# Optimization experiments

Hardware: AMD Instinct MI355X
Metric: run time of the kernel (lower is better)

Reference implementation:

```python
import jax, jax.numpy as jnp
import numpy as np

K = 10
ALPHA = 0.1
N_NODES = 100000
N_EDGES = 1600000
D_FEAT = 50


def setup_inputs() -> dict:
    key = jax.random.key(0)
    k1, k2, k3 = jax.random.split(key, 3)
    feat = jax.random.normal(k1, (N_NODES, D_FEAT), dtype=jnp.float32)
    src = jax.random.randint(k2, (N_EDGES,), 0, N_NODES, dtype=jnp.int64)
    dst = jax.random.randint(k3, (N_EDGES,), 0, N_NODES, dtype=jnp.int64)
    return {"feat": feat, "src": src, "dst": dst}


def reference(feat, src, dst):
    # APPNP: H^{t+1} = (1-a) * D^{-1/2} A D^{-1/2} H^t + a * H^0
    n = feat.shape[0]
    # in-degree per node, clipped to >= 1 (as in the original clip_by_value)
    deg = jax.ops.segment_sum(jnp.ones(dst.shape[0], feat.dtype), dst, num_segments=n)
    norm = jnp.clip(deg, 1.0, None) ** -0.5  # [N]
    norm = norm[:, None]                      # broadcast over feature dims
    feat_0 = feat
    for _ in range(K):
        h = feat * norm                       # pre-normalize (D^{-1/2})
        # message = h[src] (edge weight is 1 since edge_drop=0), aggregate by sum at dst
        agg = jax.ops.segment_sum(h[src], dst, num_segments=n)  # [N, D]
        feat = (1.0 - ALPHA) * (agg * norm) + ALPHA * feat_0
    return feat
```

## Files before the change

### kernel.cpp

```cpp
#include <hip/hip_runtime.h>
#include <hip/hip_bf16.h>


#define NN 100000
#define EE 1600000
#define DD 50
#define GS 64
#define KK 10
#define NBLK 391

__device__ __forceinline__ float feat_at(const void* f, long long i, int ft) {
    if (ft) return ((const float*)f)[i];
    unsigned int w = ((unsigned int)((const unsigned short*)f)[i]) << 16;
    return __uint_as_float(w);
}

__device__ __forceinline__ float bf16_ld(const unsigned short* p, int i) {
    unsigned int w = ((unsigned int)p[i]) << 16;
    return __uint_as_float(w);
}

__device__ __forceinline__ unsigned short bf16_st(float x) {
    unsigned int u = __float_as_uint(x);
    unsigned int r = (u + 0x7FFF + ((u >> 16) & 1)) >> 16;
    return (unsigned short)r;
}

__global__ __launch_bounds__(512) void APPNPConv_62199716381208_kernel(
        const void* featp, const void* srcp, const void* dstp,
        int* deg, float* norm, int* row_ptr, int* col_idx, int* bsum, int* flag,
        const unsigned short* gin, unsigned short* gout, float* outp,
        int phase, int last) {
    __shared__ int sh[512];
    const int tid = threadIdx.x;
    const int gidx = blockIdx.x * blockDim.x + tid;

    if (phase == 0) {
        if (gidx < NN) deg[gidx] = 0;
        if (blockIdx.x == 0 && tid == 0) {
            const int* a = (const int*)dstp;
            int odd_or = a[1] | a[3] | a[5] | a[7] | a[9] | a[11] | a[13] | a[15];
            flag[0] = (odd_or == 0) ? 1 : 0;
            const unsigned short* w = (const unsigned short*)featp;
            int isf32 = 0;
            for (int k = 0; k < 64; ++k) {
                unsigned int b = ((unsigned int)w[k]) << 16;
                float ax = fabsf(__uint_as_float(b));
                if (!(ax < 100.0f)) isf32 = 1;
            }
            flag[1] = isf32;
        }
        return;
    }
    if (phase == 1) {
        if (gidx < EE) {
            int d = flag[0] ? (int)((const long long*)dstp)[gidx]
                            : ((const int*)dstp)[gidx];
            if ((unsigned int)d < (unsigned int)NN) atomicAdd(&deg[d], 1);
        }
        return;
    }
    if (phase == 2) {
        int i = blockIdx.x * 256 + tid;
        sh[tid] = (i < NN) ? deg[i] : 0;
        __syncthreads();
        for (int off = 128; off > 0; off >>= 1) {
            if (tid < off) sh[tid] += sh[tid + off];
            __syncthreads();
        }
        if (tid == 0) bsum[blockIdx.x] = sh[0];
        return;
    }
    if (phase == 3) {
        int v = (tid < NBLK) ? bsum[tid] : 0;
        sh[tid] = v;
        __syncthreads();
        for (int off = 1; off < 512; off <<= 1) {
            int x = (tid >= off) ? sh[tid - off] : 0;
            __syncthreads();
            sh[tid] += x;
            __syncthreads();
        }
        if (tid < NBLK) bsum[tid] = sh[tid] - v;
        return;
    }
    if (phase == 4) {
        int i = blockIdx.x * 256 + tid;
        int v = (i < NN) ? deg[i] : 0;
        sh[tid] = v;
        __syncthreads();
        for (int off = 1; off < 256; off <<= 1) {
            int x = (tid >= off) ? sh[tid - off] : 0;
            __syncthreads();
            sh[tid] += x;
            __syncthreads();
        }
        int excl = sh[tid] - v + bsum[blockIdx.x];
        if (i < NN) {
            row_ptr[i] = excl;
            deg[i] = excl;
            norm[i] = rsqrtf((float)(v < 1 ? 1 : v));
        }
        if (i == 0) row_ptr[NN] = EE;
        return;
    }
    if (phase == 5) {
        if (gidx < EE) {
            int is64 = flag[0];
            int d = is64 ? (int)((const long long*)dstp)[gidx] : ((const int*)dstp)[gidx];
            int c = is64 ? (int)((const long long*)srcp)[gidx] : ((const int*)srcp)[gidx];
            if ((unsigned int)d < (unsigned int)NN && (unsigned int)c < (unsigned int)NN) {
                int pos = atomicAdd(&deg[d], 1);
                if ((unsigned int)pos < (unsigned int)EE) col_idx[pos] = c;
            }
        }
        return;
    }
    if (phase == 6) {
        int v = gidx >> 6;
        int d = gidx & 63;
        if (v < NN && d < DD) {
            float x = feat_at(featp, (long long)v * DD + d, flag[1]);
            gout[v * GS + d] = bf16_st(x * norm[v]);
        }
        return;
    }
    {
        const int lane = tid & 63;
        const int v = (blockIdx.x << 2) + (tid >> 6);
        if (v >= NN) return;
        const int beg = row_ptr[v];
        const int end = row_ptr[v + 1];
        float s0 = 0.0f, s1 = 0.0f, s2 = 0.0f, s3 = 0.0f;
        for (int base = beg; base < end; base += 64) {
            int idx = base + lane;
            int my = (idx < end) ? col_idx[idx] : 0;
            int cnt = end - base;
            if (cnt > 64) cnt = 64;
            int j = 0;
            for (; j + 8 <= cnt; j += 8) {
                int c0 = __shfl(my, j, 64);
                int c1 = __shfl(my, j + 1, 64);
                int c2 = __shfl(my, j + 2, 64);
                int c3 = __shfl(my, j + 3, 64);
                int c4 = __shfl(my, j + 4, 64);
                int c5 = __shfl(my, j + 5, 64);
                int c6 = __shfl(my, j + 6, 64);
                int c7 = __shfl(my, j + 7, 64);
                if (lane < DD) {
                    float v0 = bf16_ld(gin, c0 * GS + lane);
                    float v1 = bf16_ld(gin, c1 * GS + lane);
                    float v2 = bf16_ld(gin, c2 * GS + lane);
                    float v3 = bf16_ld(gin, c3 * GS + lane);
                    float v4 = bf16_ld(gin, c4 * GS + lane);
                    float v5 = bf16_ld(gin, c5 * GS + lane);
                    float v6 = bf16_ld(gin, c6 * GS + lane);
                    float v7 = bf16_ld(gin, c7 * GS + lane);
                    s0 += v0 + v4;
                    s1 += v1 + v5;
                    s2 += v2 + v6;
                    s3 += v3 + v7;
                }
            }
            for (; j + 4 <= cnt; j += 4) {
                int c0 = __shfl(my, j, 64);
                int c1 = __shfl(my, j + 1, 64);
                int c2 = __shfl(my, j + 2, 64);
                int c3 = __shfl(my, j + 3, 64);
                if (lane < DD) {
                    s0 += bf16_ld(gin, c0 * GS + lane);
                    s1 += bf16_ld(gin, c1 * GS + lane);
                    s2 += bf16_ld(gin, c2 * GS + lane);
                    s3 += bf16_ld(gin, c3 * GS + lane);
                }
            }
            for (; j < cnt; ++j) {
                int c = __shfl(my, j, 64);
                if (lane < DD) s0 += bf16_ld(gin, c * GS + lane);
            }
        }
        if (lane < DD) {
            float sum = (s0 + s1) + (s2 + s3);
            float nv = norm[v];
            float f0 = feat_at(featp, (long long)v * DD + lane, flag[1]);
            float res = 0.9f * (sum * nv) + 0.1f * f0;
            if (last) outp[v * DD + lane] = res;
            else      gout[v * GS + lane] = bf16_st(res * nv);
        }
    }
}

extern "C" void kernel_launch(void* const* d_in, const int* in_sizes, int n_in,
                              void* d_out, int out_size, void* d_ws, size_t ws_size,
                              hipStream_t stream) {
    const void* featp = d_in[0];
    const void* src = d_in[1];
    const void* dst = d_in[2];
    float* outf = (float*)d_out;
    unsigned short* outb16 = (unsigned short*)d_out;
    size_t out_bytes = (size_t)out_size * 4;
    (void)in_sizes;

    if (n_in != 3) {
        hipMemsetAsync(d_out, 0x50, out_bytes, stream);
        return;
    }

    size_t a_deg  = (((size_t)NN * 4) + 255) / 256 * 256;
    size_t a_norm = a_deg;
    size_t a_rp   = (((size_t)(NN + 1) * 4) + 255) / 256 * 256;
    size_t a_col  = (((size_t)EE * 4) + 255) / 256 * 256;
    size_t a_bsum = (((size_t)NBLK * 4) + 255) / 256 * 256;
    size_t a_flag = 256;
    size_t a_buf  = (((size_t)NN * GS * 2) + 255) / 256 * 256;
    if (ws_size < a_deg + a_norm + a_rp + a_col + a_bsum + a_flag + a_buf) {
        hipMemsetAsync(d_out, 0x40, out_bytes, stream);
        return;
    }
    char* p = (char*)d_ws;
    int* deg      = (int*)p;   p += a_deg;
    float* norm   = (float*)p; p += a_norm;
    int* row_ptr  = (int*)p;   p += a_rp;
    int* col_idx  = (int*)p;   p += a_col;
    int* bsum     = (int*)p;   p += a_bsum;
    int* flag     = (int*)p;   p += a_flag;
    unsigned short* bufA = (unsigned short*)p;

    (void)hipGetLastError();

    #define LCH(grid, blk, gi, go, ph, la) \
        APPNPConv_62199716381208_kernel<<<(grid), (blk), 0, stream>>>( \
            featp, src, dst, deg, norm, row_ptr, col_idx, bsum, flag, \
            (gi), (go), outf, (ph), (la))

    LCH(NBLK, 256, bufA, bufA, 0, 0);
    LCH((EE + 255) / 256, 256, bufA, bufA, 1, 0);
    LCH(NBLK, 256, bufA, bufA, 2, 0);
    LCH(1, 512, bufA, bufA, 3, 0);
    LCH(NBLK, 256, bufA, bufA, 4, 0);
    LCH((EE + 255) / 256, 256, bufA, bufA, 5, 0);
    LCH((NN * GS + 255) / 256, 256, bufA, outb16, 6, 0);

    for (int it = 1; it <= KK; ++it) {
        const unsigned short* gi = (it & 1) ? outb16 : bufA;
        unsigned short* go       = (it & 1) ? bufA : outb16;
        LCH(NN / 4, 256, gi, go, 7, (it == KK) ? 1 : 0);
    }
    #undef LCH

    if (hipGetLastError() != hipSuccess) {
        hipMemsetAsync(d_out, 0xBF, out_bytes, stream);
    }
}
```

Baseline: 804.1 us.

## Build CSR via two-level bucket sort with shared-memory histograms

```diff
diff --git a/kernel.cpp b/kernel.cpp
--- a/kernel.cpp
+++ b/kernel.cpp
@@ -7,7 +7,11 @@
 #define DD 50
 #define GS 64
 #define KK 10
-#define NBLK 391
+#define RB 9
+#define NPR 512
+#define NRANGE 196
+#define EPB 8192
+#define NPB 196
 
 __device__ __forceinline__ float feat_at(const void* f, long long i, int ft) {
     if (ft) return ((const float*)f)[i];
@@ -15,6 +19,10 @@
     return __uint_as_float(w);
 }
 
+__device__ __forceinline__ int idx_at(const void* p, int e, int is64) {
+    return is64 ? (int)((const long long*)p)[e] : ((const int*)p)[e];
+}
+
 __device__ __forceinline__ float bf16_ld(const unsigned short* p, int i) {
     unsigned int w = ((unsigned int)p[i]) << 16;
     return __uint_as_float(w);
@@ -26,18 +34,19 @@
     return (unsigned short)r;
 }
 
-__global__ __launch_bounds__(512) void APPNPConv_62199716381208_kernel(
+__global__ __launch_bounds__(256) void APPNPConv_62199716381208_kernel(
         const void* featp, const void* srcp, const void* dstp,
-        int* deg, float* norm, int* row_ptr, int* col_idx, int* bsum, int* flag,
+        float* norm, int* row_ptr, int* col_idx,
+        int* rc, int* rs, int* rcur, int* flag,
+        unsigned long long* bucket,
         const unsigned short* gin, unsigned short* gout, float* outp,
         int phase, int last) {
-    __shared__ int sh[512];
+    __shared__ int sh[1280];
     const int tid = threadIdx.x;
-    const int gidx = blockIdx.x * blockDim.x + tid;
 
     if (phase == 0) {
-        if (gidx < NN) deg[gidx] = 0;
-        if (blockIdx.x == 0 && tid == 0) {
+        if (tid < NRANGE) { rc[tid] = 0; }
+        if (tid == 0) {
             const int* a = (const int*)dstp;
             int odd_or = a[1] | a[3] | a[5] | a[7] | a[9] | a[11] | a[13] | a[15];
             flag[0] = (odd_or == 0) ? 1 : 0;
@@ -53,70 +62,114 @@
         return;
     }
     if (phase == 1) {
-        if (gidx < EE) {
-            int d = flag[0] ? (int)((const long long*)dstp)[gidx]
-                            : ((const int*)dstp)[gidx];
-            if ((unsigned int)d < (unsigned int)NN) atomicAdd(&deg[d], 1);
-        }
+        if (tid < NRANGE) sh[tid] = 0;
+        __syncthreads();
+        const int is64 = flag[0];
+        const int base_e = blockIdx.x * EPB;
+        for (int k = 0; k < EPB / 256; ++k) {
+            int e = base_e + k * 256 + tid;
+            if (e < EE) {
+                int d = idx_at(dstp, e, is64);
+                atomicAdd(&sh[d >> RB], 1);
+            }
+        }
+        __syncthreads();
+        if (tid < NRANGE && sh[tid] > 0) atomicAdd(&rc[tid], sh[tid]);
         return;
     }
     if (phase == 2) {
-        int i = blockIdx.x * 256 + tid;
-        sh[tid] = (i < NN) ? deg[i] : 0;
-        __syncthreads();
-        for (int off = 128; off > 0; off >>= 1) {
-            if (tid < off) sh[tid] += sh[tid + off];
+        int v = (tid < NRANGE) ? rc[tid] : 0;
+        sh[1024 + tid] = v;
+        __syncthreads();
+        for (int off = 1; off < 256; off <<= 1) {
+            int x = (tid >= off) ? sh[1024 + tid - off] : 0;
             __syncthreads();
-        }
-        if (tid == 0) bsum[blockIdx.x] = sh[0];
+            sh[1024 + tid] += x;
+            __syncthreads();
+        }
+        int excl = sh[1024 + tid] - v;
+        if (tid < NRANGE) { rs[tid] = excl; rcur[tid] = excl; }
+        if (tid == NRANGE) rs[NRANGE] = EE;
+        if (tid == 0) row_ptr[NN] = EE;
         return;
     }
     if (phase == 3) {
-        int v = (tid < NBLK) ? bsum[tid] : 0;
-        sh[tid] = v;
-        __syncthreads();
-        for (int off = 1; off < 512; off <<= 1) {
-            int x = (tid >= off) ? sh[tid - off] : 0;
+        if (tid < NRANGE) sh[tid] = 0;
+        __syncthreads();
+        const int is64 = flag[0];
+        const int base_e = blockIdx.x * EPB;
+        for (int k = 0; k < EPB / 256; ++k) {
+            int e = base_e + k * 256 + tid;
+            if (e < EE) {
+                int d = idx_at(dstp, e, is64);
+                atomicAdd(&sh[d >> RB], 1);
+            }
+        }
+        __syncthreads();
+        if (tid < NRANGE) {
+            sh[512 + tid] = (sh[tid] > 0) ? atomicAdd(&rcur[tid], sh[tid]) : 0;
+            sh[1024 + tid] = 0;
+        }
+        __syncthreads();
+        for (int k = 0; k < EPB / 256; ++k) {
+            int e = base_e + k * 256 + tid;
+            if (e < EE) {
+                int d = idx_at(dstp, e, is64);
+                int s = idx_at(srcp, e, is64);
+                int r = d >> RB;
+                int off = atomicAdd(&sh[1024 + r], 1);
+                bucket[sh[512 + r] + off] =
+                    (((unsigned long long)(unsigned int)d) << 32) | (unsigned int)s;
+            }
+        }
+        return;
+    }
+    if (phase == 4) {
+        const int r = blockIdx.x;
+        const int nb = r << RB;
+        const int ncnt = (NN - nb < NPR) ? (NN - nb) : NPR;
+        const int es = rs[r];
+        const int ee2 = rs[r + 1];
+        sh[tid] = 0; sh[256 + tid] = 0;
+        __syncthreads();
+        for (int e = es + tid; e < ee2; e += 256) {
+            int d = (int)(bucket[e] >> 32);
+            atomicAdd(&sh[d - nb], 1);
+        }
+        __syncthreads();
+        int a = sh[2 * tid], b = sh[2 * tid + 1];
+        int ps = a + b;
+        sh[1024 + tid] = ps;
+        __syncthreads();
+        for (int off = 1; off < 256; off <<= 1) {
+            int x = (tid >= off) ? sh[1024 + tid - off] : 0;
             __syncthreads();
-            sh[tid] += x;
+            sh[1024 + tid] += x;
             __syncthreads();
         }
-        if (tid < NBLK) bsum[tid] = sh[tid] - v;
-        return;
-    }
-    if (phase == 4) {
-        int i = blockIdx.x * 256 + tid;
-        int v = (i < NN) ? deg[i] : 0;
-        sh[tid] = v;
-        __syncthreads();
-        for (int off = 1; off < 256; off <<= 1) {
-            int x = (tid >= off) ? sh[tid - off] : 0;
-            __syncthreads();
-            sh[tid] += x;
-            __syncthreads();
-        }
-        int excl = sh[tid] - v + bsum[blockIdx.x];
-        if (i < NN) {
-            row_ptr[i] = excl;
-            deg[i] = excl;
-            norm[i] = rsqrtf((float)(v < 1 ? 1 : v));
-        }
-        if (i == 0) row_ptr[NN] = EE;
+        int exclp = sh[1024 + tid] - ps;
+        sh[512 + 2 * tid] = exclp;
+        sh[512 + 2 * tid + 1] = exclp + a;
+        __syncthreads();
+        for (int l = tid; l < NPR; l += 256) {
+            if (l < ncnt) {
+                int dg = sh[l];
+                row_ptr[nb + l] = es + sh[512 + l];
+                norm[nb + l] = rsqrtf((float)(dg < 1 ? 1 : dg));
+            }
+        }
+        __syncthreads();
+        for (int e = es + tid; e < ee2; e += 256) {
+            unsigned long long pk = bucket[e];
+            int d = (int)(pk >> 32);
+            int s = (int)(pk & 0xffffffffULL);
+            int off = atomicAdd(&sh[512 + (d - nb)], 1);
+            col_idx[es + off] = s;
+        }
         return;
     }
     if (phase == 5) {
-        if (gidx < EE) {
-            int is64 = flag[0];
-            int d = is64 ? (int)((const long long*)dstp)[gidx] : ((const int*)dstp)[gidx];
-            int c = is64 ? (int)((const long long*)srcp)[gidx] : ((const int*)srcp)[gidx];
-            if ((unsigned int)d < (unsigned int)NN && (unsigned int)c < (unsigned int)NN) {
-                int pos = atomicAdd(&deg[d], 1);
-                if ((unsigned int)pos < (unsigned int)EE) col_idx[pos] = c;
-            }
-        }
-        return;
-    }
-    if (phase == 6) {
+        int gidx = blockIdx.x * 256 + tid;
         int v = gidx >> 6;
         int d = gidx & 63;
         if (v < NN && d < DD) {
@@ -206,45 +259,46 @@
         return;
     }
 
-    size_t a_deg  = (((size_t)NN * 4) + 255) / 256 * 256;
-    size_t a_norm = a_deg;
+    size_t a_norm = (((size_t)NN * 4) + 255) / 256 * 256;
     size_t a_rp   = (((size_t)(NN + 1) * 4) + 255) / 256 * 256;
     size_t a_col  = (((size_t)EE * 4) + 255) / 256 * 256;
-    size_t a_bsum = (((size_t)NBLK * 4) + 255) / 256 * 256;
+    size_t a_rng  = (((size_t)(NRANGE + 1) * 4) + 255) / 256 * 256;
     size_t a_flag = 256;
     size_t a_buf  = (((size_t)NN * GS * 2) + 255) / 256 * 256;
-    if (ws_size < a_deg + a_norm + a_rp + a_col + a_bsum + a_flag + a_buf) {
+    size_t need = a_norm + a_rp + a_col + 3 * a_rng + a_flag + a_buf;
+    if (ws_size < need) {
         hipMemsetAsync(d_out, 0x40, out_bytes, stream);
         return;
     }
     char* p = (char*)d_ws;
-    int* deg      = (int*)p;   p += a_deg;
     float* norm   = (float*)p; p += a_norm;
     int* row_ptr  = (int*)p;   p += a_rp;
     int* col_idx  = (int*)p;   p += a_col;
-    int* bsum     = (int*)p;   p += a_bsum;
+    int* rc       = (int*)p;   p += a_rng;
+    int* rs       = (int*)p;   p += a_rng;
+    int* rcur     = (int*)p;   p += a_rng;
     int* flag     = (int*)p;   p += a_flag;
     unsigned short* bufA = (unsigned short*)p;
+    unsigned long long* bucket = (unsigned long long*)bufA;
 
     (void)hipGetLastError();
 
-    #define LCH(grid, blk, gi, go, ph, la) \
-        APPNPConv_62199716381208_kernel<<<(grid), (blk), 0, stream>>>( \
-            featp, src, dst, deg, norm, row_ptr, col_idx, bsum, flag, \
-            (gi), (go), outf, (ph), (la))
-
-    LCH(NBLK, 256, bufA, bufA, 0, 0);
-    LCH((EE + 255) / 256, 256, bufA, bufA, 1, 0);
-    LCH(NBLK, 256, bufA, bufA, 2, 0);
-    LCH(1, 512, bufA, bufA, 3, 0);
-    LCH(NBLK, 256, bufA, bufA, 4, 0);
-    LCH((EE + 255) / 256, 256, bufA, bufA, 5, 0);
-    LCH((NN * GS + 255) / 256, 256, bufA, outb16, 6, 0);
+    #define LCH(grid, gi, go, ph, la) \
+        APPNPConv_62199716381208_kernel<<<(grid), 256, 0, stream>>>( \
+            featp, src, dst, norm, row_ptr, col_idx, rc, rs, rcur, flag, \
+            bucket, (gi), (go), outf, (ph), (la))
+
+    LCH(1, bufA, bufA, 0, 0);
+    LCH(NPB, bufA, bufA, 1, 0);
+    LCH(1, bufA, bufA, 2, 0);
+    LCH(NPB, bufA, bufA, 3, 0);
+    LCH(NRANGE, bufA, bufA, 4, 0);
+    LCH((NN * GS + 255) / 256, bufA, outb16, 5, 0);
 
     for (int it = 1; it <= KK; ++it) {
         const unsigned short* gi = (it & 1) ? outb16 : bufA;
         unsigned short* go       = (it & 1) ? bufA : outb16;
-        LCH(NN / 4, 256, gi, go, 7, (it == KK) ? 1 : 0);
+        LCH(NN / 4, gi, go, 6, (it == KK) ? 1 : 0);
     }
     #undef LCH
 
```

New measurement: 810.4 us. No clear change (+0.8%).
